# Optimization experiments

Hardware: AMD Instinct MI355X
Metric: run time of the kernel (lower is better)

## Reference

```python
import jax, jax.numpy as jnp
import numpy as np

DIM = 256   # model dim (forced by gate Linear(32,4): d = 32 = DIM//H)
H = 8       # heads (hard-coded by mask.repeat(1,8,1,1))
D = DIM // H
B = 256     # batch
NS = 100    # skeleton tokens (sub-block size)
NQ = 64     # query tokens
N = NS + NQ # 164
NE = 4      # experts
HID = 50    # expert hidden
LN_EPS = 1e-5


def setup_inputs() -> dict:
    key = jax.random.key(0)
    ks = jax.random.split(key, 12)
    s = 0.02
    return {
        "x": jax.random.normal(ks[0], (B, N, DIM), jnp.float32),
        "mask": jax.random.randint(ks[1], (B, N), 0, 2).astype(bool),
        "w_qk_s": jax.random.normal(ks[2], (DIM, 2 * DIM), jnp.float32) * s,
        "w_qk_q": jax.random.normal(ks[3], (DIM, 2 * DIM), jnp.float32) * s,
        "w_v": jax.random.normal(ks[4], (DIM, DIM), jnp.float32) * s,
        "w_gate": jax.random.normal(ks[5], (D, NE), jnp.float32) * s,
        "b_gate": jnp.zeros((NE,), jnp.float32),
        "ln_gamma": jnp.ones((NE,), jnp.float32),
        "ln_beta": jnp.zeros((NE,), jnp.float32),
        "w1": jax.random.normal(ks[6], (NE, NS, HID), jnp.float32) * s,
        "b1": jnp.zeros((NE, HID), jnp.float32),
        "w2": jax.random.normal(ks[7], (NE, HID, NS), jnp.float32) * s,
        "b2": jnp.zeros((NE, NS), jnp.float32),
        "w_out": jax.random.normal(ks[8], (DIM, DIM), jnp.float32) * s,
        "b_out": jnp.zeros((DIM,), jnp.float32),
    }


def reference(x, mask, w_qk_s, w_qk_q, w_v, w_gate, b_gate, ln_gamma, ln_beta,
              w1, b1, w2, b2, w_out, b_out):
    b, n, dim = x.shape
    scale = dim ** -0.5  # scale_with_head=False -> dim**-0.5

    def to_heads(t):  # (b, m, H*D) -> (b, H, m, D)
        return t.reshape(b, -1, H, D).transpose(0, 2, 1, 3)

    # separate qk projections for skeleton (first 100) vs query (last 64) tokens
    q_s, k_s = jnp.split(x[:, :NS] @ w_qk_s, 2, axis=-1)
    q_q, k_q = jnp.split(x[:, NS:] @ w_qk_q, 2, axis=-1)
    q = jnp.concatenate([to_heads(q_s), to_heads(q_q)], axis=2)  # (b,H,N,D)
    k = jnp.concatenate([to_heads(k_s), to_heads(k_q)], axis=2)
    v = to_heads(x @ w_v)

    # gates: RAW reshape of x (b,n,H*D) -> (b,H,n,D) (memory reinterpretation,
    # as in torch x.reshape), detached, sliced to first 100 'rows'
    gx = jax.lax.stop_gradient(x).reshape(b, H, n, D)[:, :, :NS, :]
    g = gx @ w_gate + b_gate                              # (b,H,100,4)
    mu = g.mean(-1, keepdims=True)
    var = g.var(-1, keepdims=True)
    g = (g - mu) / jnp.sqrt(var + LN_EPS) * ln_gamma + ln_beta
    gates = jax.nn.softmax(g, axis=-1)                    # (b,H,100,4)

    dots = jnp.einsum('bhid,bhjd->bhij', q, k) * scale    # (b,H,N,N)
    mask_value = -jnp.finfo(dots.dtype).max
    dots = jnp.where(mask[:, None, None, :], mask_value, dots)

    # soft-MoE over the 100x100 sub-block (experts applied along key axis)
    attn_q = dots[:, :, :NS, :NS]                         # (b,H,100,100)
    h1 = jax.nn.relu(jnp.einsum('bhij,ejk->bheik', jax.nn.relu(attn_q), w1)
                     + b1[:, None, :])                    # (b,H,4,100,50)
    eo = jax.nn.relu(jnp.einsum('bheik,ekj->bheij', h1, w2)
                     + b2[:, None, :])                    # (b,H,4,100,100)
    moes = jnp.einsum('bheij,bhie->bhij', eo, gates)      # (b,H,100,100)

    dots = dots.at[:, :, :NS, :NS].add(moes)
    attn = jax.nn.softmax(dots, axis=-1)
    out = jnp.einsum('bhij,bhjd->bhid', attn, v)          # (b,H,N,D)
    out = out.transpose(0, 2, 1, 3).reshape(b, n, dim)
    return out @ w_out + b_out
```

## Files before the change

kernel.cpp:

```cpp
#include <hip/hip_runtime.h>

typedef __bf16 bf16x8 __attribute__((ext_vector_type(8)));
typedef __bf16 bf16x4 __attribute__((ext_vector_type(4)));
typedef float  f32x4  __attribute__((ext_vector_type(4)));

__device__ __forceinline__ bf16x8 ldb8(const __bf16* p) {
    return *reinterpret_cast<const bf16x8*>(p);
}
__device__ __forceinline__ bf16x8 zero8() {
    bf16x8 z;
    #pragma unroll
    for (int i = 0; i < 8; i++) z[i] = (__bf16)0.f;
    return z;
}
__device__ __forceinline__ __bf16 ldw(const void* p, int i, int m) {
    return m ? (__bf16)((const float*)p)[i] : ((const __bf16*)p)[i];
}
__device__ __forceinline__ bf16x8 ldx8(const void* p, size_t ei, int m) {
    if (m) {
        const float* f = (const float*)p + ei;
        f32x4 a = *reinterpret_cast<const f32x4*>(f);
        f32x4 b = *reinterpret_cast<const f32x4*>(f + 4);
        bf16x8 r;
        #pragma unroll
        for (int u = 0; u < 4; u++) { r[u] = (__bf16)a[u]; r[4 + u] = (__bf16)b[u]; }
        return r;
    }
    return ldb8((const __bf16*)p + ei);
}

__global__ __launch_bounds__(256) void prep_kernel(
    const void* x, const void* mask,
    const void* wqks, const void* wqkq, const void* wv, const void* w1,
    const void* w2, const void* wout, const void* wg, const void* bg,
    const void* lng, const void* lnb, const void* b1, const void* b2,
    const void* bout, int* modes, unsigned* maskb,
    __bf16* __restrict__ Wts, __bf16* __restrict__ Wtq,
    __bf16* __restrict__ w1t, __bf16* __restrict__ w2t,
    __bf16* __restrict__ wot, __bf16* __restrict__ wsm)
{
    __shared__ int sbad;
    const int t = threadIdx.x, bid = blockIdx.x;
    if (t == 0) sbad = 0;
    __syncthreads();
    {
        const unsigned int* xw = (const unsigned int*)x;
        int bad = 0;
        for (int i = t; i < 2048; i += 256) {
            unsigned int w = xw[i];
            unsigned int el = (w >> 7) & 0xFF, eh = (w >> 23) & 0xFF;
            if (el >= 0x94 || el == 0xFF) bad++;
            if (eh >= 0x94 || eh == 0xFF) bad++;
        }
        if (bad) atomicAdd(&sbad, bad);
    }
    __syncthreads();
    const int m = (sbad > 64) ? 1 : 0;

    if (bid >= 1268) {
        __shared__ int v32bad, v16bad;
        __shared__ unsigned mb[24];
        const int mbid = bid - 1268;
        if (t == 0) { v32bad = 0; v16bad = 0; }
        if (t < 24) mb[t] = ((t % 6) == 5) ? 0xFFFFFFF0u : 0u;
        __syncthreads();
        const unsigned int* mw = (const unsigned int*)mask;
        int b32 = 0, b16 = 0;
        for (int i = t; i < 10496; i += 256) {
            unsigned int w = mw[i];
            if (!(w == 0u || w == 1u || w == 0x3F800000u)) b32++;
            unsigned int h0 = w & 0xFFFFu, h1 = w >> 16;
            if (!(h0 == 0u || h0 == 1u || h0 == 0x3F80u)) b16++;
            if (!(h1 == 0u || h1 == 1u || h1 == 0x3F80u)) b16++;
        }
        if (b32) atomicAdd(&v32bad, b32);
        if (b16) atomicAdd(&v16bad, b16);
        __syncthreads();
        const int mmode = (v32bad == 0) ? 0 : ((v16bad == 0) ? 2 : 1);
        if (mbid == 0 && t == 0) { modes[0] = m; modes[1] = mmode; }
        const int lo = mbid * 656;
        for (int i2 = t; i2 < 656; i2 += 256) {
            int i = lo + i2;
            int val;
            if (mmode == 0)      val = (((const int*)mask)[i] != 0);
            else if (mmode == 2) val = (((const unsigned short*)mask)[i] != 0);
            else                 val = (((const unsigned char*)mask)[i] != 0);
            if (val) {
                int ib = i2 / 164, jb = i2 - ib * 164;
                atomicOr(&mb[ib * 6 + (jb >> 5)], 1u << (jb & 31));
            }
        }
        __syncthreads();
        if (t < 24) maskb[mbid * 24 + t] = mb[t];
        return;
    }

    int i = bid * 256 + t;
    if (i < 196608) {
        int n = i >> 8, k = i & 255;
        __bf16 vs, vq;
        if (n < 512) { vs = ldw(wqks, k * 512 + n, m); vq = ldw(wqkq, k * 512 + n, m); }
        else         { vs = ldw(wv, k * 256 + (n - 512), m); vq = vs; }
        Wts[i] = vs; Wtq[i] = vq;
        return;
    }
    i -= 196608;
    if (i < 32768) {
        int e = i >> 13, r = i & 8191, n = r >> 7, k = r & 127;
        __bf16 v = (__bf16)0.f;
        if (n < 50) {
            if (k < 100)       v = ldw(w1, (e * 100 + k) * 50 + n, m);
            else if (k == 100) v = ldw(b1, e * 50 + n, m);
        }
        w1t[i] = v;
        return;
    }
    i -= 32768;
    if (i < 28672) {
        int e = i / 7168, r = i % 7168, n = r >> 6, k = r & 63;
        __bf16 v = (__bf16)0.f;
        if (n < 100) {
            if (k < 50)       v = ldw(w2, (e * 50 + k) * 100 + n, m);
            else if (k == 50) v = ldw(b2, e * 100 + n, m);
        }
        w2t[i] = v;
        return;
    }
    i -= 28672;
    if (i < 65536) {
        int n = i >> 8, k = i & 255;
        wot[i] = ldw(wout, k * 256 + n, m);
        return;
    }
    i -= 65536;
    if (i < 996) {
        __bf16 v;
        if (i < 128)      v = ldw(wg, i, m);
        else if (i < 132) v = ldw(bg, i - 128, m);
        else if (i < 136) v = ldw(lng, i - 132, m);
        else if (i < 140) v = ldw(lnb, i - 136, m);
        else if (i < 340) v = ldw(b1, i - 140, m);
        else if (i < 740) v = ldw(b2, i - 340, m);
        else              v = ldw(bout, i - 740, m);
        wsm[i] = v;
    }
}

__global__ __launch_bounds__(256, 3) void qkv_kernel(
    const void* __restrict__ x, const __bf16* __restrict__ Wts,
    const __bf16* __restrict__ Wtq, const __bf16* __restrict__ wsm,
    const int* __restrict__ modes,
    __bf16* __restrict__ q, __bf16* __restrict__ k, __bf16* __restrict__ vt,
    float* __restrict__ gates)
{
    __shared__ __bf16 xs[32][264];
    __shared__ float wgf[128];
    __shared__ float gcst[12];
    const int m = modes[0];
    const int b = blockIdx.y;
    const int mt = blockIdx.x >> 1;
    const int half = blockIdx.x & 1;
    const __bf16* Wt = (mt < 4) ? Wts : Wtq;
    const int rbase = (mt < 4) ? mt * 32 : 100 + (mt - 4) * 32;
    const int tid = threadIdx.x;

    if (tid < 128) wgf[tid] = (float)wsm[tid];
    if (tid < 12)  gcst[tid] = (float)wsm[128 + tid];
    for (int c = tid; c < 1024; c += 256) {
        int row = c >> 5, part = c & 31;
        bf16x8 val = ldx8(x, ((size_t)b * 164 + rbase + row) * 256 + part * 8, m);
        *reinterpret_cast<bf16x8*>(&xs[row][part * 8]) = val;
    }
    __syncthreads();

    const int w = tid >> 6, l = tid & 63, lr = l & 15, lc = l >> 4;
    f32x4 acc[2][6];
    #pragma unroll
    for (int ms = 0; ms < 2; ms++)
        #pragma unroll
        for (int nt = 0; nt < 6; nt++) acc[ms][nt] = (f32x4){0.f, 0.f, 0.f, 0.f};

    #pragma unroll
    for (int kt = 0; kt < 8; kt++) {
        bf16x8 a0 = ldb8(&xs[lr][kt * 32 + lc * 8]);
        bf16x8 a1 = ldb8(&xs[16 + lr][kt * 32 + lc * 8]);
        #pragma unroll
        for (int nt = 0; nt < 6; nt++) {
            bf16x8 bb = ldb8(Wt + (size_t)(half * 384 + w * 96 + nt * 16 + lr) * 256 + kt * 32 + lc * 8);
            acc[0][nt] = __builtin_amdgcn_mfma_f32_16x16x32_bf16(a0, bb, acc[0][nt], 0, 0, 0);
            acc[1][nt] = __builtin_amdgcn_mfma_f32_16x16x32_bf16(a1, bb, acc[1][nt], 0, 0, 0);
        }
    }
    #pragma unroll
    for (int ms = 0; ms < 2; ms++) {
        #pragma unroll
        for (int nt = 0; nt < 6; nt++) {
            int c = half * 384 + w * 96 + nt * 16 + lr;
            int i0 = rbase + ms * 16 + lc * 4;
            if (c < 512) {
                __bf16* dst; int ch;
                if (c < 256) { dst = q; ch = c; }
                else         { dst = k; ch = c - 256; }
                int hh = ch >> 5, d = ch & 31;
                #pragma unroll
                for (int r = 0; r < 4; r++) {
                    int i = i0 + r;
                    if (mt >= 4 || i < 100)
                        dst[(((size_t)b * 8 + hh) * 164 + i) * 32 + d] = (__bf16)acc[ms][nt][r];
                }
            } else {
                int ch = c - 512, hh = ch >> 5, d = ch & 31;
                if (mt >= 4 || i0 < 100) {
                    bf16x4 pv;
                    #pragma unroll
                    for (int r = 0; r < 4; r++) pv[r] = (__bf16)acc[ms][nt][r];
                    *reinterpret_cast<bf16x4*>(&vt[((size_t)(b * 8 + hh) * 32 + d) * 176 + i0]) = pv;
                }
            }
        }
    }

    if ((tid >> 7) == half) {
        int jg = rbase * 8 + tid;
        int h = jg / 164;
        int j = jg - h * 164;
        if (j < 100) {
            const __bf16* xp = &xs[tid >> 3][(tid & 7) * 32];
            float g[4] = {gcst[0], gcst[1], gcst[2], gcst[3]};
            #pragma unroll
            for (int p = 0; p < 4; p++) {
                bf16x8 xv = ldb8(xp + p * 8);
                #pragma unroll
                for (int u = 0; u < 8; u++) {
                    float f = (float)xv[u];
                    #pragma unroll
                    for (int e = 0; e < 4; e++) g[e] += f * wgf[(p * 8 + u) * 4 + e];
                }
            }
            float mu = 0.25f * (g[0] + g[1] + g[2] + g[3]);
            float var = 0.25f * ((g[0]-mu)*(g[0]-mu) + (g[1]-mu)*(g[1]-mu) +
                                 (g[2]-mu)*(g[2]-mu) + (g[3]-mu)*(g[3]-mu));
            float is = rsqrtf(var + 1e-5f);
            float mx = -3.0e38f;
            #pragma unroll
            for (int e = 0; e < 4; e++) {
                g[e] = (g[e] - mu) * is * gcst[4 + e] + gcst[8 + e];
                mx = fmaxf(mx, g[e]);
            }
            float s = 0.f;
            #pragma unroll
            for (int e = 0; e < 4; e++) { g[e] = __expf(g[e] - mx); s += g[e]; }
            float inv = 1.f / s;
            float4 gv = make_float4(g[0]*inv, g[1]*inv, g[2]*inv, g[3]*inv);
            *reinterpret_cast<float4*>(&gates[((size_t)(b * 8 + h) * 100 + j) * 4]) = gv;
        }
    }
}

__global__ __launch_bounds__(256, 4) void attn_kernel(
    const __bf16* __restrict__ qg, const __bf16* __restrict__ kg,
    const __bf16* __restrict__ vtg, const float* __restrict__ gatesg,
    const unsigned* __restrict__ maskbg, const __bf16* __restrict__ w1t,
    const __bf16* __restrict__ w2t, __bf16* __restrict__ ohg)
{
    __shared__ __align__(16) __bf16 lds[19712];
    const int flat = blockIdx.x;
    const int xcd = flat & 7, j5 = flat >> 3;
    const int bh = ((j5 & 255) << 3) | xcd;
    const int rt = j5 >> 8;
    const int b = bh >> 3, tid = threadIdx.x;
    const int w = tid >> 6, l = tid & 63, lr = l & 15, lc = l >> 4;
    const int m0 = w * 16;
    const int WB  = 6400 + w * 3328;
    const int H1B = WB + 2176;
    const bool moe_wave = (rt * 64 + m0) < 100;

    const __bf16* vtb = vtg + (size_t)bh * 32 * 176;
    bf16x8 vv0, vv1, vv2;
    {
        int c = tid;
        int row = c / 24, j0 = (c - row * 24) * 8;
        if (j0 < 164) {
            vv0 = ldb8(vtb + row * 176 + j0);
            if (j0 == 160) { vv0[4] = (__bf16)0.f; vv0[5] = (__bf16)0.f; vv0[6] = (__bf16)0.f; vv0[7] = (__bf16)0.f; }
        } else vv0 = zero8();
    }
    {
        int c = tid + 256;
        int row = c / 24, j0 = (c - row * 24) * 8;
        if (j0 < 164) {
            vv1 = ldb8(vtb + row * 176 + j0);
            if (j0 == 160) { vv1[4] = (__bf16)0.f; vv1[5] = (__bf16)0.f; vv1[6] = (__bf16)0.f; vv1[7] = (__bf16)0.f; }
        } else vv1 = zero8();
    }
    {
        int c = tid + 512;
        int row = c / 24, j0 = (c - row * 24) * 8;
        if (j0 < 164) {
            vv2 = ldb8(vtb + row * 176 + j0);
            if (j0 == 160) { vv2[4] = (__bf16)0.f; vv2[5] = (__bf16)0.f; vv2[6] = (__bf16)0.f; vv2[7] = (__bf16)0.f; }
        } else vv2 = zero8();
    }

    const unsigned* mbp = maskbg + b * 6;
    unsigned mbits = 0;
    #pragma unroll
    for (int nt = 0; nt < 11; nt++)
        mbits |= ((mbp[nt >> 1] >> (((nt & 1) << 4) + lr)) & 1u) << nt;
    int qrow = rt * 64 + m0 + lr; if (qrow > 163) qrow = 163;
    bf16x8 afq = ldb8(qg + ((size_t)bh * 164 + qrow) * 32 + lc * 8);

    const __bf16* kbase = kg + (size_t)bh * 164 * 32;
    f32x4 raw[11];
    #pragma unroll
    for (int nt = 0; nt < 11; nt++) {
        int krow = nt * 16 + lr; if (krow > 163) krow = 163;
        bf16x8 kb = ldb8(kbase + (size_t)krow * 32 + lc * 8);
        f32x4 acc = {0.f, 0.f, 0.f, 0.f};
        acc = __builtin_amdgcn_mfma_f32_16x16x32_bf16(afq, kb, acc, 0, 0, 0);
        bool bad = (mbits >> nt) & 1;
        #pragma unroll
        for (int r = 0; r < 4; r++)
            raw[nt][r] = bad ? -1e30f : acc[r] * 0.0625f;
    }

    {
        int c = tid;
        int row = c / 24, j0 = (c - row * 24) * 8;
        *reinterpret_cast<bf16x8*>(&lds[row * 200 + (j0 ^ ((row & 7) << 3))]) = vv0;
        c = tid + 256;
        row = c / 24; j0 = (c - row * 24) * 8;
        *reinterpret_cast<bf16x8*>(&lds[row * 200 + (j0 ^ ((row & 7) << 3))]) = vv1;
        c = tid + 512;
        row = c / 24; j0 = (c - row * 24) * 8;
        *reinterpret_cast<bf16x8*>(&lds[row * 200 + (j0 ^ ((row & 7) << 3))]) = vv2;
    }

    if (moe_wave) {
        #pragma unroll
        for (int nt = 0; nt < 8; nt++) {
            int j = nt * 16 + lr;
            #pragma unroll
            for (int r = 0; r < 4; r++) {
                float v = raw[nt][r];
                v = (v < 0.f) ? 0.f : v;
                if (j >= 100) v = (j == 100) ? 1.f : 0.f;
                lds[WB + (lc * 4 + r) * 136 + j] = (__bf16)v;
            }
        }
    }

    if (moe_wave) {
        const int gi0 = rt * 64 + m0 + lc * 4;
        bf16x8 sa[4];
        #pragma unroll
        for (int kt = 0; kt < 4; kt++)
            sa[kt] = ldb8(&lds[WB + lr * 136 + kt * 32 + lc * 8]);
        for (int e = 0; e < 4; e++) {
            #pragma unroll
            for (int nt = 0; nt < 4; nt++) {
                f32x4 acc = {0.f, 0.f, 0.f, 0.f};
                __builtin_amdgcn_s_setprio(1);
                #pragma unroll
                for (int kt = 0; kt < 4; kt++) {
                    bf16x8 bb = ldb8(w1t + (size_t)(e * 64 + nt * 16 + lr) * 128 + kt * 32 + lc * 8);
                    acc = __builtin_amdgcn_mfma_f32_16x16x32_bf16(sa[kt], bb, acc, 0, 0, 0);
                }
                __builtin_amdgcn_s_setprio(0);
                int n = nt * 16 + lr;
                #pragma unroll
                for (int r = 0; r < 4; r++) {
                    float v = acc[r];
                    if (v < 0.f) v = 0.f;
                    if (n == 50) v = 1.f;
                    lds[H1B + (lc * 4 + r) * 72 + n] = (__bf16)v;
                }
            }
            bf16x8 ha0 = ldb8(&lds[H1B + lr * 72 + lc * 8]);
            bf16x8 ha1 = ldb8(&lds[H1B + lr * 72 + 32 + lc * 8]);
            float gt[4];
            #pragma unroll
            for (int r = 0; r < 4; r++) {
                int gi = gi0 + r;
                gt[r] = (gi < 100) ? gatesg[((size_t)bh * 100 + gi) * 4 + e] : 0.f;
            }
            #pragma unroll
            for (int nt = 0; nt < 7; nt++) {
                f32x4 acc = {0.f, 0.f, 0.f, 0.f};
                __builtin_amdgcn_s_setprio(1);
                bf16x8 bb0 = ldb8(w2t + (size_t)(e * 112 + nt * 16 + lr) * 64 + lc * 8);
                acc = __builtin_amdgcn_mfma_f32_16x16x32_bf16(ha0, bb0, acc, 0, 0, 0);
                bf16x8 bb1 = ldb8(w2t + (size_t)(e * 112 + nt * 16 + lr) * 64 + 32 + lc * 8);
                acc = __builtin_amdgcn_mfma_f32_16x16x32_bf16(ha1, bb1, acc, 0, 0, 0);
                __builtin_amdgcn_s_setprio(0);
                #pragma unroll
                for (int r = 0; r < 4; r++) {
                    float v = acc[r];
                    if (v < 0.f) v = 0.f;
                    raw[nt][r] += v * gt[r];
                }
            }
        }
    }

    float mx = -3.0e38f;
    #pragma unroll
    for (int nt = 0; nt < 11; nt++)
        #pragma unroll
        for (int r = 0; r < 4; r++) mx = fmaxf(mx, raw[nt][r]);
    const bool fast = __all(mx <= 8.f) && __any(mx > -1e29f);
    float s2v0, s2v1, s2v2, s2v3;
    #pragma unroll
    for (int r = 0; r < 4; r++) {
        float m2 = 8.f;
        if (!fast) {
            m2 = raw[0][r];
            #pragma unroll
            for (int nt = 1; nt < 11; nt++) m2 = fmaxf(m2, raw[nt][r]);
            m2 = fmaxf(m2, __shfl_xor(m2, 1, 64));
            m2 = fmaxf(m2, __shfl_xor(m2, 2, 64));
            m2 = fmaxf(m2, __shfl_xor(m2, 4, 64));
            m2 = fmaxf(m2, __shfl_xor(m2, 8, 64));
        }
        float s2 = 0.f;
        #pragma unroll
        for (int nt = 0; nt < 11; nt++) {
            float ev = __expf(raw[nt][r] - m2);
            raw[nt][r] = ev;
            s2 += ev;
        }
        s2 += __shfl_xor(s2, 1, 64);
        s2 += __shfl_xor(s2, 2, 64);
        s2 += __shfl_xor(s2, 4, 64);
        s2 += __shfl_xor(s2, 8, 64);
        if (r == 0) s2v0 = s2; else if (r == 1) s2v1 = s2;
        else if (r == 2) s2v2 = s2; else s2v3 = s2;
        const int rowp = lc * 4 + r;
        const int key = (rowp & 7) << 3;
        #pragma unroll
        for (int nt = 0; nt < 11; nt++)
            lds[WB + rowp * 200 + ((nt * 16 + lr) ^ key)] = (__bf16)raw[nt][r];
        lds[WB + rowp * 200 + ((176 + lr) ^ key)] = (__bf16)0.f;
    }
    float vsel = (lr & 3) == 0 ? s2v0 : (lr & 3) == 1 ? s2v1
               : (lr & 3) == 2 ? s2v2 : s2v3;
    float s2row = __shfl(vsel, (lr >> 2) * 16 + lr, 64);
    float invr = (s2row > 0.f) ? (1.f / s2row) : 0.f;
    __syncthreads();

    int gi = rt * 64 + m0 + lr;
    #pragma unroll
    for (int nt = 0; nt < 2; nt++) {
        f32x4 acc = {0.f, 0.f, 0.f, 0.f};
        __builtin_amdgcn_s_setprio(1);
        #pragma unroll
        for (int kt = 0; kt < 6; kt++) {
            int rowv = nt * 16 + lr;
            int col = kt * 32 + lc * 8;
            bf16x8 va = ldb8(&lds[rowv * 200 + (col ^ ((rowv & 7) << 3))]);
            bf16x8 pb = ldb8(&lds[WB + lr * 200 + (col ^ ((lr & 7) << 3))]);
            acc = __builtin_amdgcn_mfma_f32_16x16x32_bf16(va, pb, acc, 0, 0, 0);
        }
        __builtin_amdgcn_s_setprio(0);
        if (gi < 164) {
            bf16x4 ov;
            #pragma unroll
            for (int r = 0; r < 4; r++) ov[r] = (__bf16)(acc[r] * invr);
            *reinterpret_cast<bf16x4*>(&ohg[((size_t)bh * 164 + gi) * 32 + nt * 16 + lc * 4]) = ov;
        }
    }
}

__global__ __launch_bounds__(256) void outproj_kernel(
    const __bf16* __restrict__ oh, const __bf16* __restrict__ wot,
    const __bf16* __restrict__ wsm, float* __restrict__ out)
{
    const __bf16* bout = wsm + 740;
    const int b = blockIdx.y;
    const int mt = blockIdx.x >> 2;
    const int ntile = blockIdx.x & 3;
    const int tid = threadIdx.x;
    const int w = tid >> 6, l = tid & 63, lr = l & 15, lc = l >> 4;
    int row = mt * 64 + w * 16 + lr; if (row > 163) row = 163;
    f32x4 acc[4];
    #pragma unroll
    for (int nt = 0; nt < 4; nt++) acc[nt] = (f32x4){0.f, 0.f, 0.f, 0.f};
    #pragma unroll
    for (int kt = 0; kt < 8; kt++) {
        bf16x8 a = ldb8(oh + (((size_t)b * 8 + kt) * 164 + row) * 32 + lc * 8);
        #pragma unroll
        for (int nt = 0; nt < 4; nt++) {
            bf16x8 bb = ldb8(wot + (size_t)(ntile * 64 + nt * 16 + lr) * 256 + kt * 32 + lc * 8);
            acc[nt] = __builtin_amdgcn_mfma_f32_16x16x32_bf16(a, bb, acc[nt], 0, 0, 0);
        }
    }
    #pragma unroll
    for (int nt = 0; nt < 4; nt++) {
        int n = ntile * 64 + nt * 16 + lr;
        float bias = (float)bout[n];
        #pragma unroll
        for (int r = 0; r < 4; r++) {
            int i = mt * 64 + w * 16 + lc * 4 + r;
            if (i < 164)
                out[((size_t)b * 164 + i) * 256 + n] = acc[nt][r] + bias;
        }
    }
}

extern "C" void kernel_launch(void* const* d_in, const int* in_sizes, int n_in,
                              void* d_out, int out_size, void* d_ws, size_t ws_size,
                              hipStream_t stream) {
    const void* x      = d_in[0];
    const void* mask   = d_in[1];
    const void* w_qk_s = d_in[2];
    const void* w_qk_q = d_in[3];
    const void* w_v    = d_in[4];
    const void* w_gate = d_in[5];
    const void* b_gate = d_in[6];
    const void* ln_g   = d_in[7];
    const void* ln_b   = d_in[8];
    const void* w1     = d_in[9];
    const void* b1     = d_in[10];
    const void* w2     = d_in[11];
    const void* b2     = d_in[12];
    const void* w_out  = d_in[13];
    const void* b_out  = d_in[14];
    float* out = (float*)d_out;

    char* ws = (char*)d_ws;
    size_t off = 0;
    auto nextp = [&](size_t bytes) {
        char* p = ws + off;
        off += (bytes + 255) & ~(size_t)255;
        return p;
    };
    const size_t QKV_ELEMS = (size_t)256 * 8 * 164 * 32;
    const size_t VT_ELEMS  = (size_t)256 * 8 * 32 * 176;
    int*      modes  = (int*)nextp(64);
    unsigned* maskb  = (unsigned*)nextp((size_t)256 * 6 * 4);
    __bf16* qws  = (__bf16*)nextp(QKV_ELEMS * 2);
    __bf16* kws  = (__bf16*)nextp(QKV_ELEMS * 2);
    __bf16* vtws = (__bf16*)nextp(VT_ELEMS * 2);
    __bf16* ohws = (__bf16*)nextp(QKV_ELEMS * 2);
    float*  gws  = (float*)nextp((size_t)2048 * 100 * 4 * 4);
    __bf16* Wts  = (__bf16*)nextp(768 * 256 * 2);
    __bf16* Wtq  = (__bf16*)nextp(768 * 256 * 2);
    __bf16* w1t  = (__bf16*)nextp(4 * 64 * 128 * 2);
    __bf16* w2t  = (__bf16*)nextp(4 * 112 * 64 * 2);
    __bf16* wot  = (__bf16*)nextp(256 * 256 * 2);
    __bf16* wsm  = (__bf16*)nextp(996 * 2);

    prep_kernel<<<1332, 256, 0, stream>>>(x, mask, w_qk_s, w_qk_q, w_v, w1, w2,
                                          w_out, w_gate, b_gate, ln_g, ln_b, b1,
                                          b2, b_out, modes, maskb,
                                          Wts, Wtq, w1t, w2t, wot, wsm);
    qkv_kernel<<<dim3(12, 256), 256, 0, stream>>>(x, Wts, Wtq, wsm, modes,
                                                  qws, kws, vtws, gws);
    attn_kernel<<<6144, 256, 0, stream>>>(qws, kws, vtws, gws, maskb,
                                          w1t, w2t, ohws);
    outproj_kernel<<<dim3(12, 256), 256, 0, stream>>>(ohws, wot, wsm, out);
}
```

Measured before the change: 486.1 us.

## Split QKV/outproj into finer tiles with XCD-aware block mapping; drop LDS swizzle

The QKV and output-projection kernels switch to a 1-D grid of 6144 blocks, each computing a narrower column slice (quarter instead of half for QKV, 32 instead of 64 columns for outproj). Block indices are remapped so blocks that share the same batch/row tile land on the same XCD for L2 reuse, and occupancy hints are raised. Separately, the attention kernel's XOR swizzle on LDS addresses for V and probability tiles is removed in favour of plain padded indexing. The finer tiling reloads the x tile more often and repeats the staging work, and dropping the swizzle risks bank conflicts.

```diff
diff --git a/kernel.cpp b/kernel.cpp
--- a/kernel.cpp
+++ b/kernel.cpp
@@ -146,7 +146,7 @@
     }
 }
 
-__global__ __launch_bounds__(256, 3) void qkv_kernel(
+__global__ __launch_bounds__(256, 5) void qkv_kernel(
     const void* __restrict__ x, const __bf16* __restrict__ Wts,
     const __bf16* __restrict__ Wtq, const __bf16* __restrict__ wsm,
     const int* __restrict__ modes,
@@ -157,9 +157,12 @@
     __shared__ float wgf[128];
     __shared__ float gcst[12];
     const int m = modes[0];
-    const int b = blockIdx.y;
-    const int mt = blockIdx.x >> 1;
-    const int half = blockIdx.x & 1;
+    const int flat = blockIdx.x;
+    const int xcd = flat & 7, j5 = flat >> 3;
+    const int qtr = j5 / 192;
+    const int p   = xcd * 192 + (j5 - qtr * 192);
+    const int mt  = p >> 8;
+    const int b   = p & 255;
     const __bf16* Wt = (mt < 4) ? Wts : Wtq;
     const int rbase = (mt < 4) ? mt * 32 : 100 + (mt - 4) * 32;
     const int tid = threadIdx.x;
@@ -174,19 +177,20 @@
     __syncthreads();
 
     const int w = tid >> 6, l = tid & 63, lr = l & 15, lc = l >> 4;
-    f32x4 acc[2][6];
+    const int c0 = qtr * 192 + w * 48;
+    f32x4 acc[2][3];
     #pragma unroll
     for (int ms = 0; ms < 2; ms++)
         #pragma unroll
-        for (int nt = 0; nt < 6; nt++) acc[ms][nt] = (f32x4){0.f, 0.f, 0.f, 0.f};
+        for (int nt = 0; nt < 3; nt++) acc[ms][nt] = (f32x4){0.f, 0.f, 0.f, 0.f};
 
     #pragma unroll
     for (int kt = 0; kt < 8; kt++) {
         bf16x8 a0 = ldb8(&xs[lr][kt * 32 + lc * 8]);
         bf16x8 a1 = ldb8(&xs[16 + lr][kt * 32 + lc * 8]);
         #pragma unroll
-        for (int nt = 0; nt < 6; nt++) {
-            bf16x8 bb = ldb8(Wt + (size_t)(half * 384 + w * 96 + nt * 16 + lr) * 256 + kt * 32 + lc * 8);
+        for (int nt = 0; nt < 3; nt++) {
+            bf16x8 bb = ldb8(Wt + (size_t)(c0 + nt * 16 + lr) * 256 + kt * 32 + lc * 8);
             acc[0][nt] = __builtin_amdgcn_mfma_f32_16x16x32_bf16(a0, bb, acc[0][nt], 0, 0, 0);
             acc[1][nt] = __builtin_amdgcn_mfma_f32_16x16x32_bf16(a1, bb, acc[1][nt], 0, 0, 0);
         }
@@ -194,8 +198,8 @@
     #pragma unroll
     for (int ms = 0; ms < 2; ms++) {
         #pragma unroll
-        for (int nt = 0; nt < 6; nt++) {
-            int c = half * 384 + w * 96 + nt * 16 + lr;
+        for (int nt = 0; nt < 3; nt++) {
+            int c = c0 + nt * 16 + lr;
             int i0 = rbase + ms * 16 + lc * 4;
             if (c < 512) {
                 __bf16* dst; int ch;
@@ -220,7 +224,7 @@
         }
     }
 
-    if ((tid >> 7) == half) {
+    if (qtr == 0) {
         int jg = rbase * 8 + tid;
         int h = jg / 164;
         int j = jg - h * 164;
@@ -228,13 +232,13 @@
             const __bf16* xp = &xs[tid >> 3][(tid & 7) * 32];
             float g[4] = {gcst[0], gcst[1], gcst[2], gcst[3]};
             #pragma unroll
-            for (int p = 0; p < 4; p++) {
-                bf16x8 xv = ldb8(xp + p * 8);
+            for (int pp = 0; pp < 4; pp++) {
+                bf16x8 xv = ldb8(xp + pp * 8);
                 #pragma unroll
                 for (int u = 0; u < 8; u++) {
                     float f = (float)xv[u];
                     #pragma unroll
-                    for (int e = 0; e < 4; e++) g[e] += f * wgf[(p * 8 + u) * 4 + e];
+                    for (int e = 0; e < 4; e++) g[e] += f * wgf[(pp * 8 + u) * 4 + e];
                 }
             }
             float mu = 0.25f * (g[0] + g[1] + g[2] + g[3]);
@@ -327,13 +331,13 @@
     {
         int c = tid;
         int row = c / 24, j0 = (c - row * 24) * 8;
-        *reinterpret_cast<bf16x8*>(&lds[row * 200 + (j0 ^ ((row & 7) << 3))]) = vv0;
+        *reinterpret_cast<bf16x8*>(&lds[row * 200 + j0]) = vv0;
         c = tid + 256;
         row = c / 24; j0 = (c - row * 24) * 8;
-        *reinterpret_cast<bf16x8*>(&lds[row * 200 + (j0 ^ ((row & 7) << 3))]) = vv1;
+        *reinterpret_cast<bf16x8*>(&lds[row * 200 + j0]) = vv1;
         c = tid + 512;
         row = c / 24; j0 = (c - row * 24) * 8;
-        *reinterpret_cast<bf16x8*>(&lds[row * 200 + (j0 ^ ((row & 7) << 3))]) = vv2;
+        *reinterpret_cast<bf16x8*>(&lds[row * 200 + j0]) = vv2;
     }
 
     if (moe_wave) {
@@ -436,11 +440,10 @@
         if (r == 0) s2v0 = s2; else if (r == 1) s2v1 = s2;
         else if (r == 2) s2v2 = s2; else s2v3 = s2;
         const int rowp = lc * 4 + r;
-        const int key = (rowp & 7) << 3;
         #pragma unroll
         for (int nt = 0; nt < 11; nt++)
-            lds[WB + rowp * 200 + ((nt * 16 + lr) ^ key)] = (__bf16)raw[nt][r];
-        lds[WB + rowp * 200 + ((176 + lr) ^ key)] = (__bf16)0.f;
+            lds[WB + rowp * 200 + nt * 16 + lr] = (__bf16)raw[nt][r];
+        lds[WB + rowp * 200 + 176 + lr] = (__bf16)0.f;
     }
     float vsel = (lr & 3) == 0 ? s2v0 : (lr & 3) == 1 ? s2v1
                : (lr & 3) == 2 ? s2v2 : s2v3;
@@ -455,10 +458,8 @@
         __builtin_amdgcn_s_setprio(1);
         #pragma unroll
         for (int kt = 0; kt < 6; kt++) {
-            int rowv = nt * 16 + lr;
-            int col = kt * 32 + lc * 8;
-            bf16x8 va = ldb8(&lds[rowv * 200 + (col ^ ((rowv & 7) << 3))]);
-            bf16x8 pb = ldb8(&lds[WB + lr * 200 + (col ^ ((lr & 7) << 3))]);
+            bf16x8 va = ldb8(&lds[(nt * 16 + lr) * 200 + kt * 32 + lc * 8]);
+            bf16x8 pb = ldb8(&lds[WB + lr * 200 + kt * 32 + lc * 8]);
             acc = __builtin_amdgcn_mfma_f32_16x16x32_bf16(va, pb, acc, 0, 0, 0);
         }
         __builtin_amdgcn_s_setprio(0);
@@ -471,32 +472,35 @@
     }
 }
 
-__global__ __launch_bounds__(256) void outproj_kernel(
+__global__ __launch_bounds__(256, 6) void outproj_kernel(
     const __bf16* __restrict__ oh, const __bf16* __restrict__ wot,
     const __bf16* __restrict__ wsm, float* __restrict__ out)
 {
     const __bf16* bout = wsm + 740;
-    const int b = blockIdx.y;
-    const int mt = blockIdx.x >> 2;
-    const int ntile = blockIdx.x & 3;
+    const int flat = blockIdx.x;
+    const int xcd = flat & 7, j5 = flat >> 3;
+    const int ntile = j5 / 96;
+    const int p = xcd * 96 + (j5 - ntile * 96);
+    const int mt = p >> 8;
+    const int b  = p & 255;
     const int tid = threadIdx.x;
     const int w = tid >> 6, l = tid & 63, lr = l & 15, lc = l >> 4;
     int row = mt * 64 + w * 16 + lr; if (row > 163) row = 163;
-    f32x4 acc[4];
-    #pragma unroll
-    for (int nt = 0; nt < 4; nt++) acc[nt] = (f32x4){0.f, 0.f, 0.f, 0.f};
+    f32x4 acc[2];
+    #pragma unroll
+    for (int nt = 0; nt < 2; nt++) acc[nt] = (f32x4){0.f, 0.f, 0.f, 0.f};
     #pragma unroll
     for (int kt = 0; kt < 8; kt++) {
         bf16x8 a = ldb8(oh + (((size_t)b * 8 + kt) * 164 + row) * 32 + lc * 8);
         #pragma unroll
-        for (int nt = 0; nt < 4; nt++) {
-            bf16x8 bb = ldb8(wot + (size_t)(ntile * 64 + nt * 16 + lr) * 256 + kt * 32 + lc * 8);
+        for (int nt = 0; nt < 2; nt++) {
+            bf16x8 bb = ldb8(wot + (size_t)(ntile * 32 + nt * 16 + lr) * 256 + kt * 32 + lc * 8);
             acc[nt] = __builtin_amdgcn_mfma_f32_16x16x32_bf16(a, bb, acc[nt], 0, 0, 0);
         }
     }
     #pragma unroll
-    for (int nt = 0; nt < 4; nt++) {
-        int n = ntile * 64 + nt * 16 + lr;
+    for (int nt = 0; nt < 2; nt++) {
+        int n = ntile * 32 + nt * 16 + lr;
         float bias = (float)bout[n];
         #pragma unroll
         for (int r = 0; r < 4; r++) {
@@ -554,9 +558,9 @@
                                           w_out, w_gate, b_gate, ln_g, ln_b, b1,
                                           b2, b_out, modes, maskb,
                                           Wts, Wtq, w1t, w2t, wot, wsm);
-    qkv_kernel<<<dim3(12, 256), 256, 0, stream>>>(x, Wts, Wtq, wsm, modes,
-                                                  qws, kws, vtws, gws);
+    qkv_kernel<<<6144, 256, 0, stream>>>(x, Wts, Wtq, wsm, modes,
+                                         qws, kws, vtws, gws);
     attn_kernel<<<6144, 256, 0, stream>>>(qws, kws, vtws, gws, maskb,
                                           w1t, w2t, ohws);
-    outproj_kernel<<<dim3(12, 256), 256, 0, stream>>>(ohws, wot, wsm, out);
-}
+    outproj_kernel<<<6144, 256, 0, stream>>>(ohws, wot, wsm, out);
+}
```

Result: no change. 490.2 us (+0.9%).
